# Kernel tuning notes

Hardware: AMD Instinct MI355X
Metric: run time of the kernel (lower is better)

The kernel has to match this reference:

```python
import jax, jax.numpy as jnp
import numpy as np
from jax import lax

KERNEL = 2  # kernel_size, forced by the (s3-1, s4-1, s5-1) output reshape


def setup_inputs() -> dict:
    key = jax.random.key(0)
    kx, kw = jax.random.split(key)
    x = jax.random.normal(kx, (4, 16, 32, 32, 32), dtype=jnp.float32)
    w = jax.random.normal(kw, (512, 128), dtype=jnp.float32)  # (d1, d2=C*2^3)
    return {"x": x, "w": w}


def _gaussian_kernel(x, w):
    N, C, D, H, W = x.shape
    d1, d2 = w.shape
    # 3D unfold with kernel 2, stride 1, no padding -> (N, C*8, D-1, H-1, W-1)
    patches = lax.conv_general_dilated_patches(
        x,
        filter_shape=(KERNEL, KERNEL, KERNEL),
        window_strides=(1, 1, 1),
        padding='VALID',
    )
    P = (D - 1) * (H - 1) * (W - 1)
    y = patches.reshape(N, d2, P).transpose(0, 2, 1)  # (N, P, d2)
    # sum((y - w)^2) expanded as ||y||^2 - 2 y.w + ||w||^2 to avoid the
    # (N, P, d1, d2) broadcasted difference tensor.
    y_sq = jnp.sum(y * y, axis=-1, keepdims=True)           # (N, P, 1)
    w_sq = jnp.sum(w * w, axis=-1)                          # (d1,)
    cross = jnp.einsum('npd,kd->npk', y, w)                 # (N, P, d1)
    dist = y_sq - 2.0 * cross + w_sq                        # (N, P, d1)
    out = jnp.exp(-dist)
    return out.transpose(0, 2, 1).reshape(N, d1, D - 1, H - 1, W - 1)


def reference(x, w):
    return _gaussian_kernel(x, w)
```

## Files before the change

### kernel.cpp

```cpp
#include <hip/hip_runtime.h>

typedef unsigned char u8;
typedef float f32x4 __attribute__((ext_vector_type(4)));
typedef float f4u __attribute__((ext_vector_type(4), aligned(4)));

#define P_OUT 29791
#define NCH   512

__device__ __forceinline__ unsigned pk4_fp8(float a, float b, float c, float d) {
  int v = __builtin_amdgcn_cvt_pk_fp8_f32(a, b, 0, false);
  v = __builtin_amdgcn_cvt_pk_fp8_f32(c, d, v, true);
  return (unsigned)v;
}

__global__ void wprep_kernel(const float* __restrict__ w,
                             u8* __restrict__ wb, float* __restrict__ wsq) {
  const int tid = threadIdx.x;
  const int g = blockIdx.x * 16 + (tid >> 4);
  const int c = tid & 15;
  const float4* wr = (const float4*)(w + g * 128 + c * 8);
  float4 f0 = wr[0], f1 = wr[1];
  float s = f0.x*f0.x + f0.y*f0.y + f0.z*f0.z + f0.w*f0.w
          + f1.x*f1.x + f1.y*f1.y + f1.z*f1.z + f1.w*f1.w;
#pragma unroll
  for (int m = 1; m < 16; m <<= 1) s += __shfl_xor(s, m, 64);
  uint2 pk;
  pk.x = pk4_fp8(f0.x, f0.y, f0.z, f0.w);
  pk.y = pk4_fp8(f1.x, f1.y, f1.z, f1.w);
  *(uint2*)(wb + g * 128 + c * 8) = pk;
  if (c == 0) wsq[g] = s;
}

#define GLDS(g, l) __builtin_amdgcn_global_load_lds(                         \
    (const __attribute__((address_space(1))) unsigned int*)(g),              \
    (__attribute__((address_space(3))) unsigned int*)(l), 16, 0, 0)

#define LGKM_BAR() do {                                                      \
    asm volatile("s_waitcnt lgkmcnt(0)\n\ts_barrier" ::: "memory");          \
    __builtin_amdgcn_sched_barrier(0);                                       \
  } while (0)

#define VMC_BAR() do {                                                       \
    asm volatile("s_waitcnt vmcnt(16)\n\ts_barrier" ::: "memory");           \
    __builtin_amdgcn_sched_barrier(0);                                       \
  } while (0)

__global__ __launch_bounds__(256, 2)
void gauss_fused_kernel(const float* __restrict__ x,
                        const u8* __restrict__ wb,
                        const float* __restrict__ wsq,
                        float* __restrict__ out) {
  __shared__ __align__(16) u8 SMEM[66560];
  u8* Ws0 = SMEM;
  u8* Ws1 = SMEM + 16384;
  float* Xs = (float*)(SMEM + 32768);
  float* Ep = (float*)(SMEM + 32768);

  const int bid = blockIdx.x;
  const int tile = (bid & 7) * 124 + (bid >> 3);
  const unsigned nb = (unsigned)tile / 248u;
  const unsigned r2 = (unsigned)tile - nb * 248u;
  const unsigned d  = r2 >> 3;
  const unsigned hb = r2 & 7;
  const int h0 = hb * 4;
  const int nh = (h0 + 4 <= 31) ? 4 : (31 - h0);
  const int nrows = nh * 31;
  const int tp0 = d * 961 + h0 * 31;

  const int tid = threadIdx.x;
  const int wid = tid >> 6;
  const int lane = tid & 63;
  const int quad = lane >> 4;
  const int col = lane & 15;
  const int wch = wid & 1;
  const int wp = wid >> 1;

#pragma unroll
  for (int t = 0; t < 4; ++t) {
    const int Lb = (wid * 4 + t) * 64;
    const int L = Lb + lane;
    const int row = L >> 3;
    const int jc = (L & 7) ^ (row & 7);
    GLDS(wb + (size_t)row * 128 + jc * 16, &Ws0[Lb * 16]);
  }

#pragma unroll
  for (int t = 0; t < 6; ++t) {
    if (t < 5 || wid == 0) {
      const int Lb = t * 256 + wid * 64;
      const int L = Lb + lane;
      unsigned c = (unsigned)L / 82u;
      if (c > 15u) c = 15u;
      unsigned rc = (unsigned)L - c * 82u;
      if (rc > 79u) rc = 79u;
      const unsigned kd = rc / 40u;
      const unsigned rr = rc - kd * 40u;
      const unsigned hq = rr >> 3;
      const int jc = (int)(rr & 7u);
      const int hg = h0 + (int)hq;
      const int hcl = (hg < 31) ? hg : 31;
      GLDS(x + (((size_t)(nb * 16 + c)) << 15) + (d + kd) * 1024 + hcl * 32 + jc * 4,
           &Xs[Lb * 4]);
    }
  }

  int rb[4];
  int xoff[4];
#pragma unroll
  for (int j = 0; j < 4; ++j) {
    rb[j] = wp * 64 + j * 16 + col;
    const unsigned rc = (unsigned)((rb[j] < nrows) ? rb[j] : (nrows - 1));
    const unsigned hh = rc / 31u;
    const unsigned wv = rc - hh * 31u;
    xoff[j] = (int)(hh * 32 + wv);
  }

  __syncthreads();

#pragma unroll
  for (int t = 0; t < 4; ++t) {
    const int Lb = (wid * 4 + t) * 64;
    const int L = Lb + lane;
    const int row = L >> 3;
    const int jc = (L & 7) ^ (row & 7);
    GLDS(wb + (size_t)(128 + row) * 128 + jc * 16, &Ws1[Lb * 16]);
  }

  long long B[4][4];
  float sq[4] = {0.f, 0.f, 0.f, 0.f};
#pragma unroll
  for (int ks = 0; ks < 4; ++ks) {
    const int cc = ks * 4 + quad;
    const float* xb = &Xs[cc * 328];
#pragma unroll
    for (int j = 0; j < 4; ++j) {
      const float* pB = xb + xoff[j];
      const float v0 = pB[0],   v1 = pB[1],   v2 = pB[32],  v3 = pB[33];
      const float v4 = pB[160], v5 = pB[161], v6 = pB[192], v7 = pB[193];
      sq[j] += v0*v0 + v1*v1 + v2*v2 + v3*v3 + v4*v4 + v5*v5 + v6*v6 + v7*v7;
      const unsigned lo = pk4_fp8(v0, v1, v2, v3);
      const unsigned hi = pk4_fp8(v4, v5, v6, v7);
      B[ks][j] = (long long)(((unsigned long long)hi << 32) | lo);
    }
  }
#pragma unroll
  for (int j = 0; j < 4; ++j) {
    sq[j] += __shfl_xor(sq[j], 16, 64);
    sq[j] += __shfl_xor(sq[j], 32, 64);
  }

  const int c16b = quad >> 1;
  const int hoff = (quad & 1) * 8;
  const int hw = lane >> 5;
  const int ll = lane & 31;
  const int nfull = (nrows == 124) ? 31 : 23;

#pragma unroll
  for (int ct = 0; ct < 4; ++ct) {
    if (ct > 0) VMC_BAR();
    const u8* Wcur = (ct & 1) ? Ws1 : Ws0;

    f32x4 acc[4][4];
#pragma unroll
    for (int i = 0; i < 4; ++i)
#pragma unroll
      for (int j = 0; j < 4; ++j) acc[i][j] = (f32x4){0.f, 0.f, 0.f, 0.f};

#pragma unroll
    for (int ks = 0; ks < 4; ++ks) {
      long long a[4];
#pragma unroll
      for (int i = 0; i < 4; ++i) {
        const int rowA = wch * 64 + i * 16 + col;
        const int pa = (ks * 2 + c16b) ^ (rowA & 7);
        a[i] = *(const long long*)&Wcur[rowA * 128 + pa * 16 + hoff];
      }
#pragma unroll
      for (int i = 0; i < 4; ++i)
#pragma unroll
        for (int j = 0; j < 4; ++j)
          acc[i][j] = __builtin_amdgcn_mfma_f32_16x16x32_fp8_fp8(a[i], B[ks][j],
                                                                 acc[i][j], 0, 0, 0);
    }

    LGKM_BAR();

    if (ct < 2) {
      u8* Wn = (ct & 1) ? Ws1 : Ws0;
      const int cb = (ct + 2) * 128;
#pragma unroll
      for (int t = 0; t < 4; ++t) {
        const int Lb = (wid * 4 + t) * 64;
        const int L = Lb + lane;
        const int row = L >> 3;
        const int jc = (L & 7) ^ (row & 7);
        GLDS(wb + (size_t)(cb + row) * 128 + jc * 16, &Wn[Lb * 16]);
      }
    }

    const int c0 = ct * 128;
#pragma unroll
    for (int pa = 0; pa < 2; ++pa) {
#pragma unroll
      for (int ii = 0; ii < 2; ++ii) {
        const int i = pa * 2 + ii;
#pragma unroll
        for (int r = 0; r < 4; ++r) {
          const int ch2 = wch * 32 + ii * 16 + quad * 4 + r;
          const int chl = wch * 64 + pa * 32 + ii * 16 + quad * 4 + r;
          const float wsv = wsq[c0 + chl];
#pragma unroll
          for (int j = 0; j < 4; ++j)
            Ep[ch2 * 132 + rb[j]] = __expf(2.f * acc[i][j][r] - sq[j] - wsv);
        }
      }
      LGKM_BAR();

#pragma unroll
      for (int rr = 0; rr < 8; ++rr) {
        const int ch2 = wid * 16 + rr * 2 + hw;
        const int chl = (ch2 >> 5) * 64 + pa * 32 + (ch2 & 31);
        float* ob = out + ((size_t)(nb * NCH + c0 + chl)) * P_OUT + tp0;
        if (ll < nfull) {
          const f4u v = *(const f4u*)&Ep[ch2 * 132 + 4 * ll];
          *(f4u*)(ob + 4 * ll) = v;
        } else if (ll == 23 && nrows == 93) {
          ob[92] = Ep[ch2 * 132 + 92];
        }
      }
      if (pa == 0) LGKM_BAR();
    }
  }
}

extern "C" void kernel_launch(void* const* d_in, const int* in_sizes, int n_in,
                              void* d_out, int out_size, void* d_ws, size_t ws_size,
                              hipStream_t stream) {
  const float* x = (const float*)d_in[0];
  const float* w = (const float*)d_in[1];
  float* out = (float*)d_out;
  char* ws = (char*)d_ws;
  u8* wb     = (u8*)ws;
  float* wsq = (float*)(ws + 65536);

  wprep_kernel<<<32, 256, 0, stream>>>(w, wb, wsq);
  gauss_fused_kernel<<<992, 256, 0, stream>>>(x, wb, wsq, out);
}
```

Baseline: 251.6 us.

## Shrink LDS footprint by quartering epilogue staging and compacting X tile

The epilogue now stages 32 channels at a time in four phases instead of 64 channels in two. The X tile is stored without per-channel padding (320 floats per channel instead of 328), loaded in five uniform iterations. Together these cut shared memory from 66560 to 53248 bytes, which could let a third block fit per CU if register usage allows. The cost is extra barriers and more store phases in the epilogue.

Measured after the change: 260.7 us. +3.6%, slower.

```diff
diff --git a/kernel.cpp b/kernel.cpp
--- a/kernel.cpp
+++ b/kernel.cpp
@@ -50,7 +50,7 @@
                         const u8* __restrict__ wb,
                         const float* __restrict__ wsq,
                         float* __restrict__ out) {
-  __shared__ __align__(16) u8 SMEM[66560];
+  __shared__ __align__(16) u8 SMEM[53248];
   u8* Ws0 = SMEM;
   u8* Ws1 = SMEM + 16384;
   float* Xs = (float*)(SMEM + 32768);
@@ -85,23 +85,19 @@
   }
 
 #pragma unroll
-  for (int t = 0; t < 6; ++t) {
-    if (t < 5 || wid == 0) {
-      const int Lb = t * 256 + wid * 64;
-      const int L = Lb + lane;
-      unsigned c = (unsigned)L / 82u;
-      if (c > 15u) c = 15u;
-      unsigned rc = (unsigned)L - c * 82u;
-      if (rc > 79u) rc = 79u;
-      const unsigned kd = rc / 40u;
-      const unsigned rr = rc - kd * 40u;
-      const unsigned hq = rr >> 3;
-      const int jc = (int)(rr & 7u);
-      const int hg = h0 + (int)hq;
-      const int hcl = (hg < 31) ? hg : 31;
-      GLDS(x + (((size_t)(nb * 16 + c)) << 15) + (d + kd) * 1024 + hcl * 32 + jc * 4,
-           &Xs[Lb * 4]);
-    }
+  for (int t = 0; t < 5; ++t) {
+    const int Lb = t * 256 + wid * 64;
+    const int L = Lb + lane;
+    const int row = L >> 3;
+    const int jc = L & 7;
+    const unsigned c = (unsigned)row / 10u;
+    const unsigned rr = (unsigned)row - c * 10u;
+    const unsigned kd = rr / 5u;
+    const unsigned hq = rr - kd * 5u;
+    const int hg = h0 + (int)hq;
+    const int hcl = (hg < 31) ? hg : 31;
+    GLDS(x + (((size_t)(nb * 16 + c)) << 15) + (d + kd) * 1024 + hcl * 32 + jc * 4,
+         &Xs[Lb * 4]);
   }
 
   int rb[4];
@@ -131,7 +127,7 @@
 #pragma unroll
   for (int ks = 0; ks < 4; ++ks) {
     const int cc = ks * 4 + quad;
-    const float* xb = &Xs[cc * 328];
+    const float* xb = &Xs[cc * 320];
 #pragma unroll
     for (int j = 0; j < 4; ++j) {
       const float* pB = xb + xoff[j];
@@ -200,26 +196,23 @@
 
     const int c0 = ct * 128;
 #pragma unroll
-    for (int pa = 0; pa < 2; ++pa) {
-#pragma unroll
-      for (int ii = 0; ii < 2; ++ii) {
-        const int i = pa * 2 + ii;
-#pragma unroll
-        for (int r = 0; r < 4; ++r) {
-          const int ch2 = wch * 32 + ii * 16 + quad * 4 + r;
-          const int chl = wch * 64 + pa * 32 + ii * 16 + quad * 4 + r;
-          const float wsv = wsq[c0 + chl];
-#pragma unroll
-          for (int j = 0; j < 4; ++j)
-            Ep[ch2 * 132 + rb[j]] = __expf(2.f * acc[i][j][r] - sq[j] - wsv);
-        }
+    for (int q = 0; q < 4; ++q) {
+      const int q2 = q >> 1, q1 = q & 1;
+#pragma unroll
+      for (int r = 0; r < 4; ++r) {
+        const int ch2 = wch * 16 + quad * 4 + r;
+        const int chl = wch * 64 + q2 * 32 + q1 * 16 + quad * 4 + r;
+        const float wsv = wsq[c0 + chl];
+#pragma unroll
+        for (int j = 0; j < 4; ++j)
+          Ep[ch2 * 132 + rb[j]] = __expf(2.f * acc[q][j][r] - sq[j] - wsv);
       }
       LGKM_BAR();
 
 #pragma unroll
-      for (int rr = 0; rr < 8; ++rr) {
-        const int ch2 = wid * 16 + rr * 2 + hw;
-        const int chl = (ch2 >> 5) * 64 + pa * 32 + (ch2 & 31);
+      for (int rr = 0; rr < 4; ++rr) {
+        const int ch2 = wid * 8 + rr * 2 + hw;
+        const int chl = (ch2 >> 4) * 64 + q2 * 32 + q1 * 16 + (ch2 & 15);
         float* ob = out + ((size_t)(nb * NCH + c0 + chl)) * P_OUT + tp0;
         if (ll < nfull) {
           const f4u v = *(const f4u*)&Ep[ch2 * 132 + 4 * ll];
@@ -228,7 +221,7 @@
           ob[92] = Ep[ch2 * 132 + 92];
         }
       }
-      if (pa == 0) LGKM_BAR();
+      if (q < 3) LGKM_BAR();
     }
   }
 }
```

## Double-buffer epilogue staging to overlap exp writes with global stores

Applied to the files above, without the earlier changes.

The epilogue now splits each 128-channel tile into four 32-channel slices staged through two ping-pong LDS buffers. The global store of one slice is interleaved with the exp computation and LDS write of the next, which cuts the barriers per tile from four to four smaller ones and removes the write-after-read barrier. The intent is to overlap store issue with exp math and reduce the time waves sit idle at barriers. In exchange there are more, smaller store bursts, and the final slice's store is not covered by any overlap.

New measurement: 254.1 us. Within noise of the previous version (+1.0%).

```diff
diff --git a/kernel.cpp b/kernel.cpp
--- a/kernel.cpp
+++ b/kernel.cpp
@@ -199,36 +199,69 @@
     }
 
     const int c0 = ct * 128;
-#pragma unroll
-    for (int pa = 0; pa < 2; ++pa) {
-#pragma unroll
-      for (int ii = 0; ii < 2; ++ii) {
-        const int i = pa * 2 + ii;
+    {
+      float* Epd = Ep;
+#pragma unroll
+      for (int r = 0; r < 4; ++r) {
+        const int ch2 = wch * 16 + quad * 4 + r;
+        const int chl = wch * 64 + quad * 4 + r;
+        const float wsv = wsq[c0 + chl];
+#pragma unroll
+        for (int j = 0; j < 4; ++j)
+          Epd[ch2 * 132 + rb[j]] = __expf(2.f * acc[0][j][r] - sq[j] - wsv);
+      }
+    }
+    LGKM_BAR();
+
+#pragma unroll
+    for (int q = 1; q < 4; ++q) {
+      {
+        const int qs = q - 1;
+        const float* Eps = Ep + (qs & 1) * 4224;
+        const int s2 = qs >> 1, s1 = qs & 1;
+#pragma unroll
+        for (int rr = 0; rr < 4; ++rr) {
+          const int ch2 = wid * 8 + rr * 2 + hw;
+          const int chl = (ch2 >> 4) * 64 + s2 * 32 + s1 * 16 + (ch2 & 15);
+          float* ob = out + ((size_t)(nb * NCH + c0 + chl)) * P_OUT + tp0;
+          if (ll < nfull) {
+            const f4u v = *(const f4u*)&Eps[ch2 * 132 + 4 * ll];
+            *(f4u*)(ob + 4 * ll) = v;
+          } else if (ll == 23 && nrows == 93) {
+            ob[92] = Eps[ch2 * 132 + 92];
+          }
+        }
+      }
+      {
+        float* Epd = Ep + (q & 1) * 4224;
+        const int q2 = q >> 1, q1 = q & 1;
 #pragma unroll
         for (int r = 0; r < 4; ++r) {
-          const int ch2 = wch * 32 + ii * 16 + quad * 4 + r;
-          const int chl = wch * 64 + pa * 32 + ii * 16 + quad * 4 + r;
+          const int ch2 = wch * 16 + quad * 4 + r;
+          const int chl = wch * 64 + q2 * 32 + q1 * 16 + quad * 4 + r;
           const float wsv = wsq[c0 + chl];
 #pragma unroll
           for (int j = 0; j < 4; ++j)
-            Ep[ch2 * 132 + rb[j]] = __expf(2.f * acc[i][j][r] - sq[j] - wsv);
+            Epd[ch2 * 132 + rb[j]] = __expf(2.f * acc[q][j][r] - sq[j] - wsv);
         }
       }
       LGKM_BAR();
-
-#pragma unroll
-      for (int rr = 0; rr < 8; ++rr) {
-        const int ch2 = wid * 16 + rr * 2 + hw;
-        const int chl = (ch2 >> 5) * 64 + pa * 32 + (ch2 & 31);
+    }
+
+    {
+      const float* Eps = Ep + 4224;
+#pragma unroll
+      for (int rr = 0; rr < 4; ++rr) {
+        const int ch2 = wid * 8 + rr * 2 + hw;
+        const int chl = (ch2 >> 4) * 64 + 32 + 16 + (ch2 & 15);
         float* ob = out + ((size_t)(nb * NCH + c0 + chl)) * P_OUT + tp0;
         if (ll < nfull) {
-          const f4u v = *(const f4u*)&Ep[ch2 * 132 + 4 * ll];
+          const f4u v = *(const f4u*)&Eps[ch2 * 132 + 4 * ll];
           *(f4u*)(ob + 4 * ll) = v;
         } else if (ll == 23 && nrows == 93) {
-          ob[92] = Ep[ch2 * 132 + 92];
+          ob[92] = Eps[ch2 * 132 + 92];
         }
       }
-      if (pa == 0) LGKM_BAR();
     }
   }
 }
```
